# Optimization experiments

Measured on AMD Instinct MI355X. Metric: run time of the kernel, lower is better.

Reference implementation:

```python
import jax, jax.numpy as jnp
import numpy as np

EPS = 1e-5
NUM_HEADS = 4

# Spiking neuron: single-timestep LIF with threshold 1.0 (Heaviside forward,
# ATan surrogate gradient as in snntorch's default spike_grad).
@jax.custom_vjp
def spike(v):
    return (v >= 1.0).astype(v.dtype)

def _spike_fwd(v):
    return spike(v), v

def _spike_bwd(v, g):
    u = v - 1.0
    return (g / (1.0 + (jnp.pi * u) ** 2),)

spike.defvjp(_spike_fwd, _spike_bwd)

def layernorm(x, g, b):
    mu = jnp.mean(x, axis=-1, keepdims=True)
    var = jnp.var(x, axis=-1, keepdims=True)
    return (x - mu) * jax.lax.rsqrt(var + EPS) * g + b

def batchnorm(x, g, b):
    # BatchNorm1d applied on (B, C, N) == per-channel stats over (B, N) of (B, N, C)
    mu = jnp.mean(x, axis=(0, 1))
    var = jnp.var(x, axis=(0, 1))
    return (x - mu) * jax.lax.rsqrt(var + EPS) * g + b

def lin_bn_spike(x, w, g, b):
    # Linear (no bias) -> BatchNorm1d -> spiking neuron
    return spike(batchnorm(jnp.einsum('bnc,oc->bno', x, w), g, b))


def setup_inputs() -> dict:
    key = jax.random.key(0)
    ks = jax.random.split(key, 8)
    B, N, C = 8, 2048, 256
    Hid = 1024  # int(256 * 4.0)
    s = 0.02
    d = {
        'x': jax.random.normal(ks[0], (B, N, C), jnp.float32),
        'ln1_g': jnp.ones((C,), jnp.float32), 'ln1_b': jnp.zeros((C,), jnp.float32),
        'wq': jax.random.normal(ks[1], (C, C), jnp.float32) * s,
        'q_g': jnp.ones((C,), jnp.float32), 'q_b': jnp.zeros((C,), jnp.float32),
        'wk': jax.random.normal(ks[2], (C, C), jnp.float32) * s,
        'k_g': jnp.ones((C,), jnp.float32), 'k_b': jnp.zeros((C,), jnp.float32),
        'wv': jax.random.normal(ks[3], (C, C), jnp.float32) * s,
        'v_g': jnp.ones((C,), jnp.float32), 'v_b': jnp.zeros((C,), jnp.float32),
        'wo': jax.random.normal(ks[4], (C, C), jnp.float32) * s,
        'ln2_g': jnp.ones((C,), jnp.float32), 'ln2_b': jnp.zeros((C,), jnp.float32),
        'w1': jax.random.normal(ks[5], (Hid, C), jnp.float32) * s,
        'bn1_g': jnp.ones((Hid,), jnp.float32), 'bn1_b': jnp.zeros((Hid,), jnp.float32),
        'w2': jax.random.normal(ks[6], (C, Hid), jnp.float32) * s,
        'bn2_g': jnp.ones((C,), jnp.float32), 'bn2_b': jnp.zeros((C,), jnp.float32),
    }
    return d


def reference(x, ln1_g, ln1_b, wq, q_g, q_b, wk, k_g, k_b, wv, v_g, v_b, wo,
              ln2_g, ln2_b, w1, bn1_g, bn1_b, w2, bn2_g, bn2_b):
    B, N, C = x.shape
    H = NUM_HEADS
    D = C // H
    scale = D ** (-0.5)

    # --- Spiking self-attention on norm1(x) ---
    h = layernorm(x, ln1_g, ln1_b)
    q = lin_bn_spike(h, wq, q_g, q_b)
    k = lin_bn_spike(h, wk, k_g, k_b)
    v = lin_bn_spike(h, wv, v_g, v_b)
    qh = q.reshape(B, N, H, D).transpose(0, 2, 1, 3)
    kh = k.reshape(B, N, H, D).transpose(0, 2, 1, 3)
    vh = v.reshape(B, N, H, D).transpose(0, 2, 1, 3)
    attn = jnp.einsum('bhnd,bhmd->bhnm', qh, kh) * scale  # no softmax
    o = jnp.einsum('bhnm,bhmd->bhnd', attn, vh)
    o = o.transpose(0, 2, 1, 3).reshape(B, N, C)
    x = x + jnp.einsum('bnc,oc->bno', o, wo)

    # --- Spiking MLP on norm2(x) (dropout=0.0) ---
    h = layernorm(x, ln2_g, ln2_b)
    m = lin_bn_spike(h, w1, bn1_g, bn1_b)
    m = lin_bn_spike(m, w2, bn2_g, bn2_b)
    return x + m
```

## Files before the change

### kernel.cpp

```cpp
#include <hip/hip_runtime.h>
#include <cstddef>
#include <cstdint>

#define RR 16384
#define CC 256
#define NN 2048

typedef __attribute__((ext_vector_type(8))) _Float16 h8;
typedef __attribute__((ext_vector_type(4))) float float4v;
typedef unsigned short u16;

__device__ inline float h2f(u16 u) {
  return (float)__builtin_bit_cast(_Float16, u);
}
__device__ inline u16 f2h(float f) {
  return __builtin_bit_cast(u16, (_Float16)f);
}

__global__ __launch_bounds__(256) void ln_split(const float* __restrict__ x,
    const float* __restrict__ g, const float* __restrict__ b,
    u16* __restrict__ out) {
  const int wave = threadIdx.x >> 6, lane = threadIdx.x & 63;
  const int row = (blockIdx.x << 2) + wave;
  const float4 v = ((const float4*)(x + (size_t)row * CC))[lane];
  float s1 = v.x + v.y + v.z + v.w;
  float s2 = v.x * v.x + v.y * v.y + v.z * v.z + v.w * v.w;
#pragma unroll
  for (int o = 32; o > 0; o >>= 1) {
    s1 += __shfl_xor(s1, o);
    s2 += __shfl_xor(s2, o);
  }
  const float mu = s1 * (1.0f / CC);
  const float var = s2 * (1.0f / CC) - mu * mu;
  const float rs = 1.0f / sqrtf(var + 1e-5f);
  const float4 gg = ((const float4*)g)[lane];
  const float4 bb = ((const float4*)b)[lane];
  float o4[4];
  o4[0] = (v.x - mu) * rs * gg.x + bb.x;
  o4[1] = (v.y - mu) * rs * gg.y + bb.y;
  o4[2] = (v.z - mu) * rs * gg.z + bb.z;
  o4[3] = (v.w - mu) * rs * gg.w + bb.w;
  ushort4 hi, lo;
  hi.x = f2h(o4[0]); lo.x = f2h(o4[0] - h2f(hi.x));
  hi.y = f2h(o4[1]); lo.y = f2h(o4[1] - h2f(hi.y));
  hi.z = f2h(o4[2]); lo.z = f2h(o4[2] - h2f(hi.z));
  hi.w = f2h(o4[3]); lo.w = f2h(o4[3] - h2f(hi.w));
  *(ushort4*)(out + (size_t)row * 512 + (lane << 2)) = hi;
  *(ushort4*)(out + (size_t)row * 512 + 256 + (lane << 2)) = lo;
}

__global__ __launch_bounds__(256) void split_all(const float* __restrict__ wq,
    const float* __restrict__ wk, const float* __restrict__ wv,
    const float* __restrict__ wo, const float* __restrict__ w1,
    const float* __restrict__ w2, u16* __restrict__ Wqkv,
    u16* __restrict__ wo2, u16* __restrict__ w12, u16* __restrict__ w22) {
  const int bid = blockIdx.x;
  if (bid < 768) {
    const float* W = (bid < 256) ? wq : (bid < 512) ? wk : wv;
    const int rowoff = (bid >> 8) << 8;
    const int li = (bid & 255) * 256 + threadIdx.x;
    const int o = li >> 8, k = li & 255;
    const float w = W[li];
    const u16 h1 = f2h(w);
    const u16 h2 = f2h(w - h2f(h1));
    u16* base = Wqkv + (size_t)(o + rowoff) * 768;
    base[k] = h1; base[256 + k] = h1; base[512 + k] = h2;
  } else if (bid < 1024) {
    const int li = (bid - 768) * 256 + threadIdx.x;
    wo2[li] = f2h(wo[li]);
  } else if (bid < 2048) {
    const int li = (bid - 1024) * 256 + threadIdx.x;
    w12[li] = f2h(w1[li]);
  } else {
    const int li = (bid - 2048) * 256 + threadIdx.x;
    w22[li] = f2h(w2[li]);
  }
}

template <int BM, int BN, int WM, int WN, int STATS, int MINW, int OUTF16,
          int LNFUSE>
__global__ __launch_bounds__(512, MINW) void gemm_sp(
    const u16* __restrict__ A, int AW,
    const u16* __restrict__ W2, int K2,
    const float* __restrict__ resid, void* __restrict__ Yv, int O,
    float* __restrict__ p1, float* __restrict__ p2,
    const float* __restrict__ lng, const float* __restrict__ lnb,
    u16* __restrict__ h2out) {
  constexpr int FM = BM / (WM * 16);
  constexpr int FN = BN / (WN * 16);
  constexpr int LA = BM / 64;
  constexpr int LB = BN / 64;
  constexpr int NL = LA + LB;
  static_assert(WM * WN == 8, "8 waves");
  static_assert(NL == 3 || NL == 4 || NL == 5 || NL == 7 || NL == 8,
                "vmcnt literal");
  static_assert(!LNFUSE || (BM == 64 && BN == 256), "LNFUSE tile");
  __shared__ __align__(16) u16 As[2][BM * 64];
  __shared__ __align__(16) u16 Bs[2][BN * 64];
  const int tid = threadIdx.x;
  const int lane = tid & 63, wid = tid >> 6;
  const int wr = wid / WN, wc = wid % WN;
  const int gx = gridDim.x;
  const int lid = blockIdx.y * gx + blockIdx.x;
  const int chunk = (gx * gridDim.y) >> 3;
  const int nid = (lid & 7) * chunk + (lid >> 3);
  const int bx = nid % gx, by = nid / gx;
  const int r0 = by * BM, o0 = bx * BN;
  const int lrow = tid >> 3;
  const int lce = ((tid & 7) ^ ((tid >> 3) & 7)) << 3;

  auto STAGE = [&](int buf, int kAs, int k0s) {
#pragma unroll
    for (int i = 0; i < LA; ++i) {
      const u16* srcA = A + (size_t)(r0 + i * 64 + lrow) * AW + kAs + lce;
      __builtin_amdgcn_global_load_lds(
          (const __attribute__((address_space(1))) void*)srcA,
          (__attribute__((address_space(3))) void*)&As[buf][(i * 64 + wid * 8) * 64],
          16, 0, 0);
    }
#pragma unroll
    for (int i = 0; i < LB; ++i) {
      const u16* srcB = W2 + (size_t)(o0 + i * 64 + lrow) * K2 + k0s + lce;
      __builtin_amdgcn_global_load_lds(
          (const __attribute__((address_space(1))) void*)srcB,
          (__attribute__((address_space(3))) void*)&Bs[buf][(i * 64 + wid * 8) * 64],
          16, 0, 0);
    }
  };

  float4v acc[FM][FN] = {};
  STAGE(0, 0, 0);
  int kA = 0, cur = 0;
  for (int k0 = 0; k0 < K2; k0 += 64) {
    const int kAn = (kA + 64) & (AW - 1);
    if (k0 + 64 < K2) {
      STAGE(cur ^ 1, kAn, k0 + 64);
      if constexpr (NL == 3)
        asm volatile("s_waitcnt vmcnt(3)\n\ts_barrier" ::: "memory");
      else if constexpr (NL == 4)
        asm volatile("s_waitcnt vmcnt(4)\n\ts_barrier" ::: "memory");
      else if constexpr (NL == 5)
        asm volatile("s_waitcnt vmcnt(5)\n\ts_barrier" ::: "memory");
      else if constexpr (NL == 7)
        asm volatile("s_waitcnt vmcnt(7)\n\ts_barrier" ::: "memory");
      else
        asm volatile("s_waitcnt vmcnt(8)\n\ts_barrier" ::: "memory");
    } else {
      asm volatile("s_waitcnt vmcnt(0)\n\ts_barrier" ::: "memory");
    }
#pragma unroll
    for (int kk = 0; kk < 2; ++kk) {
      h8 a[FM], b[FN];
      const int ch0 = (kk << 2) + (lane >> 4);
      const int chs = ch0 ^ (lane & 7);
#pragma unroll
      for (int m = 0; m < FM; ++m) {
        const int R = wr * (FM * 16) + m * 16 + (lane & 15);
        a[m] = *(const h8*)&As[cur][R * 64 + chs * 8];
      }
#pragma unroll
      for (int n = 0; n < FN; ++n) {
        const int Rb = wc * (FN * 16) + n * 16 + (lane & 15);
        b[n] = *(const h8*)&Bs[cur][Rb * 64 + chs * 8];
      }
#pragma unroll
      for (int m = 0; m < FM; ++m)
#pragma unroll
        for (int n = 0; n < FN; ++n)
          acc[m][n] = __builtin_amdgcn_mfma_f32_16x16x32_f16(a[m], b[n], acc[m][n], 0, 0, 0);
    }
    asm volatile("s_waitcnt lgkmcnt(0)\n\ts_barrier" ::: "memory");
    kA = kAn; cur ^= 1;
  }
  const int crow = (lane >> 4) << 2, ccol = lane & 15;
  float* ft = (float*)Bs;
#pragma unroll
  for (int m = 0; m < FM; ++m)
#pragma unroll
    for (int n = 0; n < FN; ++n)
#pragma unroll
      for (int j = 0; j < 4; ++j) {
        const int lr = wr * (FM * 16) + (m << 4) + crow + j;
        const int lc = wc * (FN * 16) + (n << 4) + ccol;
        const size_t idx = (size_t)(r0 + lr) * O + o0 + lc;
        float v = acc[m][n][j];
        if constexpr (OUTF16) {
          ((u16*)Yv)[idx] = f2h(v);
        } else {
          if (resid) v += resid[idx];
          ((float*)Yv)[idx] = v;
        }
        if constexpr (LNFUSE) ft[lr * 256 + lc] = v;
      }
  if constexpr (LNFUSE) {
    __syncthreads();
    const int rr0 = wid << 3;
    const float4 gg = ((const float4*)lng)[lane];
    const float4 bb = ((const float4*)lnb)[lane];
#pragma unroll
    for (int rr = 0; rr < 8; ++rr) {
      const int r = rr0 + rr;
      const float4 v = ((const float4*)ft)[r * 64 + lane];
      float s1 = v.x + v.y + v.z + v.w;
      float s2 = v.x * v.x + v.y * v.y + v.z * v.z + v.w * v.w;
#pragma unroll
      for (int o = 32; o > 0; o >>= 1) {
        s1 += __shfl_xor(s1, o);
        s2 += __shfl_xor(s2, o);
      }
      const float mu = s1 * (1.0f / CC);
      const float var = s2 * (1.0f / CC) - mu * mu;
      const float rs = 1.0f / sqrtf(var + 1e-5f);
      ushort4 hh;
      hh.x = f2h((v.x - mu) * rs * gg.x + bb.x);
      hh.y = f2h((v.y - mu) * rs * gg.y + bb.y);
      hh.z = f2h((v.z - mu) * rs * gg.z + bb.z);
      hh.w = f2h((v.w - mu) * rs * gg.w + bb.w);
      *(ushort4*)(h2out + (size_t)(r0 + r) * 256 + (lane << 2)) = hh;
    }
  }
  if (STATS) {
    float s1[FN], s2[FN];
#pragma unroll
    for (int n = 0; n < FN; ++n) {
      s1[n] = 0.f; s2[n] = 0.f;
#pragma unroll
      for (int m = 0; m < FM; ++m)
#pragma unroll
        for (int j = 0; j < 4; ++j) {
          const float v = acc[m][n][j];
          s1[n] += v; s2[n] += v * v;
        }
    }
#pragma unroll
    for (int n = 0; n < FN; ++n) {
      s1[n] += __shfl_xor(s1[n], 16); s1[n] += __shfl_xor(s1[n], 32);
      s2[n] += __shfl_xor(s2[n], 16); s2[n] += __shfl_xor(s2[n], 32);
    }
    float* sb = (float*)As;
    __syncthreads();
    if (lane < 16) {
#pragma unroll
      for (int n = 0; n < FN; ++n) {
        const int cl = wc * (FN * 16) + n * 16 + lane;
        sb[wr * BN + cl] = s1[n];
        sb[WM * BN + wr * BN + cl] = s2[n];
      }
    }
    __syncthreads();
    if (tid < BN) {
      float a = 0.f, b = 0.f;
#pragma unroll
      for (int w = 0; w < WM; ++w) {
        a += sb[w * BN + tid];
        b += sb[WM * BN + w * BN + tid];
      }
      p1[(size_t)by * O + o0 + tid] = a;
      p2[(size_t)by * O + o0 + tid] = b;
    }
  }
}

__global__ __launch_bounds__(256) void bn_stats2(const float* __restrict__ p1,
    const float* __restrict__ p2, float* __restrict__ mu,
    float* __restrict__ rinv, int O, int npanels) {
  const int c0 = blockIdx.x << 6;
  const int c = threadIdx.x & 63;
  const int jg = threadIdx.x >> 6;
  float s1 = 0.f, s2 = 0.f;
#pragma unroll 4
  for (int j = jg; j < npanels; j += 4) {
    s1 += p1[(size_t)j * O + c0 + c];
    s2 += p2[(size_t)j * O + c0 + c];
  }
  __shared__ float sb[8][64];
  sb[jg][c] = s1;
  sb[4 + jg][c] = s2;
  __syncthreads();
  if (threadIdx.x < 64) {
    const float a = ((sb[0][c] + sb[1][c]) + (sb[2][c] + sb[3][c]));
    const float b = ((sb[4][c] + sb[5][c]) + (sb[6][c] + sb[7][c]));
    const float m = a * (1.0f / 16384.f);
    const float v = b * (1.0f / 16384.f) - m * m;
    mu[c0 + c] = m;
    rinv[c0 + c] = 1.0f / sqrtf(v + 1e-5f);
  }
}

__global__ __launch_bounds__(256) void bn_spike_h16(const u16* __restrict__ Y,
    const float* __restrict__ mu, const float* __restrict__ rinv,
    const float* __restrict__ g, const float* __restrict__ b,
    u16* __restrict__ S, int O) {
  const int i = blockIdx.x * 256 + threadIdx.x;
  const int c = (i << 2) & (O - 1);
  const ushort4 yh = ((const ushort4*)Y)[i];
  const float4 m4 = *(const float4*)(mu + c);
  const float4 r4 = *(const float4*)(rinv + c);
  const float4 g4 = *(const float4*)(g + c);
  const float4 b4 = *(const float4*)(b + c);
  ushort4 s;
  s.x = ((h2f(yh.x) - m4.x) * r4.x * g4.x + b4.x >= 1.0f) ? (u16)0x3C00 : (u16)0;
  s.y = ((h2f(yh.y) - m4.y) * r4.y * g4.y + b4.y >= 1.0f) ? (u16)0x3C00 : (u16)0;
  s.z = ((h2f(yh.z) - m4.z) * r4.z * g4.z + b4.z >= 1.0f) ? (u16)0x3C00 : (u16)0;
  s.w = ((h2f(yh.w) - m4.w) * r4.w * g4.w + b4.w >= 1.0f) ? (u16)0x3C00 : (u16)0;
  ((ushort4*)S)[i] = s;
}

__global__ __launch_bounds__(256) void bn_spike_add_h16(
    const u16* __restrict__ Y, const float* __restrict__ mu,
    const float* __restrict__ rinv, const float* __restrict__ g,
    const float* __restrict__ b, float* __restrict__ addOut, int O) {
  const int i = blockIdx.x * 256 + threadIdx.x;
  const int c = (i << 2) & (O - 1);
  const ushort4 yh = ((const ushort4*)Y)[i];
  const float4 m4 = *(const float4*)(mu + c);
  const float4 r4 = *(const float4*)(rinv + c);
  const float4 g4 = *(const float4*)(g + c);
  const float4 b4 = *(const float4*)(b + c);
  float4 o4 = ((const float4*)addOut)[i];
  o4.x += ((h2f(yh.x) - m4.x) * r4.x * g4.x + b4.x >= 1.0f) ? 1.0f : 0.0f;
  o4.y += ((h2f(yh.y) - m4.y) * r4.y * g4.y + b4.y >= 1.0f) ? 1.0f : 0.0f;
  o4.z += ((h2f(yh.z) - m4.z) * r4.z * g4.z + b4.z >= 1.0f) ? 1.0f : 0.0f;
  o4.w += ((h2f(yh.w) - m4.w) * r4.w * g4.w + b4.w >= 1.0f) ? 1.0f : 0.0f;
  ((float4*)addOut)[i] = o4;
}

__global__ __launch_bounds__(256) void attn_kv(const float* __restrict__ Yq,
    const float* __restrict__ mu, const float* __restrict__ rinv,
    const float* __restrict__ kg, const float* __restrict__ kb,
    const float* __restrict__ vg, const float* __restrict__ vb,
    float* __restrict__ Mpart) {
  const int bh = blockIdx.x, sp = blockIdx.y;
  const int b = bh >> 2, h = bh & 3;
  const int t = threadIdx.x;
  const int gq = t >> 6, e = t & 63;
  __shared__ float ks[16][64], vs[16][64];
  float acc[16] = {};
  const int lrow = t >> 4, lf = (t & 15) << 2;
  const int c = (h << 6) + lf;
  const int ck = 256 + c, cv = 512 + c;
  const float4 kmu = *(const float4*)(mu + ck);
  const float4 krv = *(const float4*)(rinv + ck);
  const float4 kg4 = *(const float4*)(kg + c);
  const float4 kb4 = *(const float4*)(kb + c);
  const float4 vmu = *(const float4*)(mu + cv);
  const float4 vrv = *(const float4*)(rinv + cv);
  const float4 vg4 = *(const float4*)(vg + c);
  const float4 vb4 = *(const float4*)(vb + c);
  for (int n0 = sp * 128; n0 < sp * 128 + 128; n0 += 16) {
    const size_t rowb = (size_t)(b * NN + n0 + lrow) * 768;
    const float4 kq = *(const float4*)(Yq + rowb + ck);
    const float4 vq = *(const float4*)(Yq + rowb + cv);
    __syncthreads();
    ks[lrow][lf + 0] = ((kq.x - kmu.x) * krv.x * kg4.x + kb4.x >= 1.0f) ? 1.f : 0.f;
    ks[lrow][lf + 1] = ((kq.y - kmu.y) * krv.y * kg4.y + kb4.y >= 1.0f) ? 1.f : 0.f;
    ks[lrow][lf + 2] = ((kq.z - kmu.z) * krv.z * kg4.z + kb4.z >= 1.0f) ? 1.f : 0.f;
    ks[lrow][lf + 3] = ((kq.w - kmu.w) * krv.w * kg4.w + kb4.w >= 1.0f) ? 1.f : 0.f;
    vs[lrow][lf + 0] = ((vq.x - vmu.x) * vrv.x * vg4.x + vb4.x >= 1.0f) ? 1.f : 0.f;
    vs[lrow][lf + 1] = ((vq.y - vmu.y) * vrv.y * vg4.y + vb4.y >= 1.0f) ? 1.f : 0.f;
    vs[lrow][lf + 2] = ((vq.z - vmu.z) * vrv.z * vg4.z + vb4.z >= 1.0f) ? 1.f : 0.f;
    vs[lrow][lf + 3] = ((vq.w - vmu.w) * vrv.w * vg4.w + vb4.w >= 1.0f) ? 1.f : 0.f;
    __syncthreads();
#pragma unroll
    for (int nn = 0; nn < 16; ++nn) {
      const float vv = vs[nn][e];
#pragma unroll
      for (int i = 0; i < 16; ++i) acc[i] += ks[nn][(gq << 4) + i] * vv;
    }
  }
  float* mp = Mpart + ((size_t)bh * 16 + sp) * 4096;
#pragma unroll
  for (int i = 0; i < 16; ++i) mp[((gq << 4) + i) * 64 + e] = acc[i];
}

__global__ __launch_bounds__(256) void attn_kv_reduce(
    const float* __restrict__ Mpart, float* __restrict__ M) {
  const int i = blockIdx.x * 256 + threadIdx.x;
  const int bh = i >> 12, j = i & 4095;
  float s = 0.f;
#pragma unroll
  for (int sp = 0; sp < 16; ++sp)
    s += Mpart[((size_t)bh * 16 + sp) * 4096 + j];
  M[i] = s;
}

__global__ __launch_bounds__(256) void attn_qm(const float* __restrict__ Yq,
    const float* __restrict__ mu, const float* __restrict__ rinv,
    const float* __restrict__ qg, const float* __restrict__ qb,
    const float* __restrict__ M, u16* __restrict__ O1) {
  const int h = blockIdx.x;
  const int r0 = blockIdx.y << 6;
  const int b = blockIdx.y >> 5;
  const int t = threadIdx.x;
  const int e = t & 63, rg = t >> 6;
  __shared__ float Ms[64][64];
  __shared__ float qs[64][64];
  const float* Mb = M + ((size_t)(b * 4 + h) << 12);
  for (int i = t; i < 4096; i += 256) ((float*)Ms)[i] = Mb[i];
  const int c = (h << 6) + e;
  const float qmu = mu[c], qrv = rinv[c], qgg = qg[c], qbb = qb[c];
  for (int rl = rg; rl < 64; rl += 4) {
    const float y = Yq[(size_t)(r0 + rl) * 768 + c];
    qs[rl][e] = ((y - qmu) * qrv * qgg + qbb >= 1.0f) ? 1.f : 0.f;
  }
  __syncthreads();
  for (int rl = rg; rl < 64; rl += 4) {
    float acc = 0.f;
#pragma unroll
    for (int d = 0; d < 64; ++d) acc += qs[rl][d] * Ms[d][e];
    O1[(size_t)(r0 + rl) * 256 + (h << 6) + e] = f2h(0.125f * acc);
  }
}

extern "C" void kernel_launch(void* const* d_in, const int* in_sizes, int n_in,
                              void* d_out, int out_size, void* d_ws,
                              size_t ws_size, hipStream_t stream) {
  const float* x    = (const float*)d_in[0];
  const float* ln1g = (const float*)d_in[1];
  const float* ln1b = (const float*)d_in[2];
  const float* wq   = (const float*)d_in[3];
  const float* qg   = (const float*)d_in[4];
  const float* qb   = (const float*)d_in[5];
  const float* wk   = (const float*)d_in[6];
  const float* kg   = (const float*)d_in[7];
  const float* kb   = (const float*)d_in[8];
  const float* wv   = (const float*)d_in[9];
  const float* vg   = (const float*)d_in[10];
  const float* vb   = (const float*)d_in[11];
  const float* wo   = (const float*)d_in[12];
  const float* ln2g = (const float*)d_in[13];
  const float* ln2b = (const float*)d_in[14];
  const float* w1   = (const float*)d_in[15];
  const float* b1g  = (const float*)d_in[16];
  const float* b1b  = (const float*)d_in[17];
  const float* w2   = (const float*)d_in[18];
  const float* b2g  = (const float*)d_in[19];
  const float* b2b  = (const float*)d_in[20];
  float* out = (float*)d_out;
  char* ws = (char*)d_ws;
  const size_t MB = 1u << 20;
  u16*   h1s   = (u16*)(ws);
  float* Yq    = (float*)(ws + 16 * MB);
  float* Mpart = (float*)(ws + 88 * MB);
  float* Mful  = (float*)(ws + 96 * MB);
  u16*   o16   = (u16*)(ws);
  u16*   h2_16 = (u16*)(ws + 16 * MB);
  u16*   Ym16  = (u16*)(ws + 32 * MB);
  u16*   Y2    = (u16*)(ws + 64 * MB);
  u16*   m1    = (u16*)(ws + 97 * MB);
  u16*   Wqkv  = (u16*)(ws + 129 * MB);
  u16*   wo2   = (u16*)(ws + 131 * MB);
  u16*   w12   = (u16*)(ws + 132 * MB);
  u16*   w22   = (u16*)(ws + 134 * MB);
  float* p1    = (float*)(ws + 135 * MB);
  float* p2    = (float*)(ws + 136 * MB);
  float* mu    = (float*)(ws + 137 * MB);
  float* rinv  = (float*)(ws + 137 * MB + 32768);

  const dim3 blk(256);
  const dim3 blk512(512);

  split_all<<<3072, blk, 0, stream>>>(wq, wk, wv, wo, w1, w2, Wqkv, wo2, w12, w22);

  ln_split<<<RR / 4, blk, 0, stream>>>(x, ln1g, ln1b, h1s);

  gemm_sp<128, 192, 2, 4, 1, 4, 0, 0><<<dim3(4, 128), blk512, 0, stream>>>(
      h1s, 512, Wqkv, 768, nullptr, Yq, 768, p1, p2, nullptr, nullptr, nullptr);

  bn_stats2<<<12, blk, 0, stream>>>(p1, p2, mu, rinv, 768, 128);

  attn_kv<<<dim3(32, 16), blk, 0, stream>>>(Yq, mu, rinv, kg, kb, vg, vb, Mpart);
  attn_kv_reduce<<<512, blk, 0, stream>>>(Mpart, Mful);
  attn_qm<<<dim3(4, RR / 64), blk, 0, stream>>>(Yq, mu, rinv, qg, qb, Mful, o16);

  gemm_sp<64, 256, 2, 4, 0, 4, 0, 1><<<dim3(1, 256), blk512, 0, stream>>>(
      o16, 256, wo2, 256, x, out, 256, nullptr, nullptr, ln2g, ln2b, h2_16);

  gemm_sp<128, 128, 2, 4, 1, 4, 1, 0><<<dim3(8, 128), blk512, 0, stream>>>(
      h2_16, 256, w12, 256, nullptr, Ym16, 1024, p1, p2, nullptr, nullptr,
      nullptr);
  bn_stats2<<<16, blk, 0, stream>>>(p1, p2, mu, rinv, 1024, 128);
  bn_spike_h16<<<16384, blk, 0, stream>>>(Ym16, mu, rinv, b1g, b1b, m1, 1024);

  gemm_sp<64, 128, 2, 4, 1, 4, 1, 0><<<dim3(2, 256), blk512, 0, stream>>>(
      m1, 1024, w22, 1024, nullptr, Y2, 256, p1, p2, nullptr, nullptr, nullptr);
  bn_stats2<<<4, blk, 0, stream>>>(p1, p2, mu, rinv, 256, 256);
  bn_spike_add_h16<<<4096, blk, 0, stream>>>(Y2, mu, rinv, b2g, b2b, out, 256);
}
```

Measured before the change: 172.8 us.

## Fuse BN1+spike into MLP second GEMM A-tile load path

Removes the standalone bn_spike_h16 pass over the 16384x1024 hidden activations. The second MLP GEMM now reads the fp16 pre-BN outputs and applies the folded per-channel scale/shift plus threshold while staging A into LDS. bn_stats2 is extended to precompute the scale and shift so the fused path needs only one FMA per element. This saves a full read and write of a 32MB intermediate and one launch, at the cost of extra ALU work and register pressure inside the GEMM's A-load path, which now goes through registers instead of direct-to-LDS.

```diff
diff --git a/kernel.cpp b/kernel.cpp
--- a/kernel.cpp
+++ b/kernel.cpp
@@ -8,6 +8,7 @@
 
 typedef __attribute__((ext_vector_type(8))) _Float16 h8;
 typedef __attribute__((ext_vector_type(4))) float float4v;
+typedef __attribute__((ext_vector_type(8))) unsigned short u16x8;
 typedef unsigned short u16;
 
 __device__ inline float h2f(u16 u) {
@@ -261,9 +262,160 @@
   }
 }
 
+__global__ __launch_bounds__(512, 4) void gemm_mlp2f(
+    const u16* __restrict__ A, const u16* __restrict__ W2,
+    const float* __restrict__ sc, const float* __restrict__ sh,
+    u16* __restrict__ Y, float* __restrict__ p1, float* __restrict__ p2) {
+  constexpr int BM = 64, BN = 128, WM = 2, WN = 4, K2 = 1024;
+  constexpr int FM = 2, FN = 2;
+  __shared__ __align__(16) u16 As[2][BM * 64];
+  __shared__ __align__(16) u16 Bs[2][BN * 64];
+  const int tid = threadIdx.x;
+  const int lane = tid & 63, wid = tid >> 6;
+  const int wr = wid / WN, wc = wid % WN;
+  const int gx = gridDim.x;
+  const int lid = blockIdx.y * gx + blockIdx.x;
+  const int chunk = (gx * gridDim.y) >> 3;
+  const int nid = (lid & 7) * chunk + (lid >> 3);
+  const int bx = nid % gx, by = nid / gx;
+  const int r0 = by * BM, o0 = bx * BN;
+  const int lrow = tid >> 3;
+  const int cs = (tid & 7) ^ (lrow & 7);
+
+  u16x8 a1, a2;
+  float4 c01, c11, s01, s11, c02, c12, s02, s12;
+  auto LOADA = [&](int k0s, u16x8& av, float4& c0, float4& c1, float4& s0,
+                   float4& s1) {
+    av = *(const u16x8*)(A + (size_t)(r0 + lrow) * 1024 + k0s + cs * 8);
+    const int ch = k0s + cs * 8;
+    c0 = *(const float4*)(sc + ch);
+    c1 = *(const float4*)(sc + ch + 4);
+    s0 = *(const float4*)(sh + ch);
+    s1 = *(const float4*)(sh + ch + 4);
+  };
+  auto STAGE_B = [&](int buf, int k0s) {
+#pragma unroll
+    for (int i = 0; i < 2; ++i) {
+      const u16* srcB = W2 + (size_t)(o0 + i * 64 + lrow) * K2 + k0s +
+                        (((tid & 7) ^ (lrow & 7)) << 3);
+      __builtin_amdgcn_global_load_lds(
+          (const __attribute__((address_space(1))) void*)srcB,
+          (__attribute__((address_space(3))) void*)&Bs[buf][(i * 64 + wid * 8) * 64],
+          16, 0, 0);
+    }
+  };
+  auto WRITEA = [&](int buf, u16x8 av, float4 c0, float4 c1, float4 s0,
+                    float4 s1) {
+    u16x8 sp;
+    sp[0] = (h2f(av[0]) * c0.x + s0.x >= 1.0f) ? (u16)0x3C00 : (u16)0;
+    sp[1] = (h2f(av[1]) * c0.y + s0.y >= 1.0f) ? (u16)0x3C00 : (u16)0;
+    sp[2] = (h2f(av[2]) * c0.z + s0.z >= 1.0f) ? (u16)0x3C00 : (u16)0;
+    sp[3] = (h2f(av[3]) * c0.w + s0.w >= 1.0f) ? (u16)0x3C00 : (u16)0;
+    sp[4] = (h2f(av[4]) * c1.x + s1.x >= 1.0f) ? (u16)0x3C00 : (u16)0;
+    sp[5] = (h2f(av[5]) * c1.y + s1.y >= 1.0f) ? (u16)0x3C00 : (u16)0;
+    sp[6] = (h2f(av[6]) * c1.z + s1.z >= 1.0f) ? (u16)0x3C00 : (u16)0;
+    sp[7] = (h2f(av[7]) * c1.w + s1.w >= 1.0f) ? (u16)0x3C00 : (u16)0;
+    *(u16x8*)&As[buf][lrow * 64 + (tid & 7) * 8] = sp;
+  };
+
+  float4v acc[FM][FN] = {};
+  LOADA(0, a1, c01, c11, s01, s11);
+  STAGE_B(0, 0);
+  int cur = 0;
+  for (int k0 = 0; k0 < K2; k0 += 64) {
+    if (k0 + 64 < K2) {
+      LOADA(k0 + 64, a2, c02, c12, s02, s12);
+      STAGE_B(cur ^ 1, k0 + 64);
+      asm volatile("s_waitcnt vmcnt(7)\n\ts_barrier" ::: "memory");
+    } else {
+      asm volatile("s_waitcnt vmcnt(0)\n\ts_barrier" ::: "memory");
+    }
+    WRITEA(cur, a1, c01, c11, s01, s11);
+    asm volatile("s_waitcnt lgkmcnt(0)\n\ts_barrier" ::: "memory");
+#pragma unroll
+    for (int kk = 0; kk < 2; ++kk) {
+      h8 a[FM], b[FN];
+      const int ch0 = (kk << 2) + (lane >> 4);
+      const int chs = ch0 ^ (lane & 7);
+#pragma unroll
+      for (int m = 0; m < FM; ++m) {
+        const int R = wr * 32 + m * 16 + (lane & 15);
+        a[m] = *(const h8*)&As[cur][R * 64 + chs * 8];
+      }
+#pragma unroll
+      for (int n = 0; n < FN; ++n) {
+        const int Rb = wc * 32 + n * 16 + (lane & 15);
+        b[n] = *(const h8*)&Bs[cur][Rb * 64 + chs * 8];
+      }
+#pragma unroll
+      for (int m = 0; m < FM; ++m)
+#pragma unroll
+        for (int n = 0; n < FN; ++n)
+          acc[m][n] = __builtin_amdgcn_mfma_f32_16x16x32_f16(a[m], b[n], acc[m][n], 0, 0, 0);
+    }
+    asm volatile("s_waitcnt lgkmcnt(0)\n\ts_barrier" ::: "memory");
+    cur ^= 1;
+    a1 = a2; c01 = c02; c11 = c12; s01 = s02; s11 = s12;
+  }
+  const int crow = (lane >> 4) << 2, ccol = lane & 15;
+#pragma unroll
+  for (int m = 0; m < FM; ++m)
+#pragma unroll
+    for (int n = 0; n < FN; ++n)
+#pragma unroll
+      for (int j = 0; j < 4; ++j) {
+        const size_t idx =
+            (size_t)(r0 + wr * 32 + (m << 4) + crow + j) * 256 +
+            o0 + wc * 32 + (n << 4) + ccol;
+        Y[idx] = f2h(acc[m][n][j]);
+      }
+  {
+    float s1[FN], s2[FN];
+#pragma unroll
+    for (int n = 0; n < FN; ++n) {
+      s1[n] = 0.f; s2[n] = 0.f;
+#pragma unroll
+      for (int m = 0; m < FM; ++m)
+#pragma unroll
+        for (int j = 0; j < 4; ++j) {
+          const float v = acc[m][n][j];
+          s1[n] += v; s2[n] += v * v;
+        }
+    }
+#pragma unroll
+    for (int n = 0; n < FN; ++n) {
+      s1[n] += __shfl_xor(s1[n], 16); s1[n] += __shfl_xor(s1[n], 32);
+      s2[n] += __shfl_xor(s2[n], 16); s2[n] += __shfl_xor(s2[n], 32);
+    }
+    float* sb = (float*)As;
+    __syncthreads();
+    if (lane < 16) {
+#pragma unroll
+      for (int n = 0; n < FN; ++n) {
+        const int cl = wc * 32 + n * 16 + lane;
+        sb[wr * BN + cl] = s1[n];
+        sb[WM * BN + wr * BN + cl] = s2[n];
+      }
+    }
+    __syncthreads();
+    if (tid < BN) {
+      float a = 0.f, b = 0.f;
+#pragma unroll
+      for (int w = 0; w < WM; ++w) {
+        a += sb[w * BN + tid];
+        b += sb[WM * BN + w * BN + tid];
+      }
+      p1[(size_t)by * 256 + o0 + tid] = a;
+      p2[(size_t)by * 256 + o0 + tid] = b;
+    }
+  }
+}
+
 __global__ __launch_bounds__(256) void bn_stats2(const float* __restrict__ p1,
     const float* __restrict__ p2, float* __restrict__ mu,
-    float* __restrict__ rinv, int O, int npanels) {
+    float* __restrict__ rinv, int O, int npanels,
+    const float* __restrict__ g, const float* __restrict__ b,
+    float* __restrict__ sc, float* __restrict__ sh) {
   const int c0 = blockIdx.x << 6;
   const int c = threadIdx.x & 63;
   const int jg = threadIdx.x >> 6;
@@ -279,31 +431,18 @@
   __syncthreads();
   if (threadIdx.x < 64) {
     const float a = ((sb[0][c] + sb[1][c]) + (sb[2][c] + sb[3][c]));
-    const float b = ((sb[4][c] + sb[5][c]) + (sb[6][c] + sb[7][c]));
+    const float bb = ((sb[4][c] + sb[5][c]) + (sb[6][c] + sb[7][c]));
     const float m = a * (1.0f / 16384.f);
-    const float v = b * (1.0f / 16384.f) - m * m;
+    const float v = bb * (1.0f / 16384.f) - m * m;
+    const float rv = 1.0f / sqrtf(v + 1e-5f);
     mu[c0 + c] = m;
-    rinv[c0 + c] = 1.0f / sqrtf(v + 1e-5f);
-  }
-}
-
-__global__ __launch_bounds__(256) void bn_spike_h16(const u16* __restrict__ Y,
-    const float* __restrict__ mu, const float* __restrict__ rinv,
-    const float* __restrict__ g, const float* __restrict__ b,
-    u16* __restrict__ S, int O) {
-  const int i = blockIdx.x * 256 + threadIdx.x;
-  const int c = (i << 2) & (O - 1);
-  const ushort4 yh = ((const ushort4*)Y)[i];
-  const float4 m4 = *(const float4*)(mu + c);
-  const float4 r4 = *(const float4*)(rinv + c);
-  const float4 g4 = *(const float4*)(g + c);
-  const float4 b4 = *(const float4*)(b + c);
-  ushort4 s;
-  s.x = ((h2f(yh.x) - m4.x) * r4.x * g4.x + b4.x >= 1.0f) ? (u16)0x3C00 : (u16)0;
-  s.y = ((h2f(yh.y) - m4.y) * r4.y * g4.y + b4.y >= 1.0f) ? (u16)0x3C00 : (u16)0;
-  s.z = ((h2f(yh.z) - m4.z) * r4.z * g4.z + b4.z >= 1.0f) ? (u16)0x3C00 : (u16)0;
-  s.w = ((h2f(yh.w) - m4.w) * r4.w * g4.w + b4.w >= 1.0f) ? (u16)0x3C00 : (u16)0;
-  ((ushort4*)S)[i] = s;
+    rinv[c0 + c] = rv;
+    if (sc) {
+      const float scale = rv * g[c0 + c];
+      sc[c0 + c] = scale;
+      sh[c0 + c] = b[c0 + c] - m * scale;
+    }
+  }
 }
 
 __global__ __launch_bounds__(256) void bn_spike_add_h16(
@@ -447,7 +586,6 @@
   u16*   h2_16 = (u16*)(ws + 16 * MB);
   u16*   Ym16  = (u16*)(ws + 32 * MB);
   u16*   Y2    = (u16*)(ws + 64 * MB);
-  u16*   m1    = (u16*)(ws + 97 * MB);
   u16*   Wqkv  = (u16*)(ws + 129 * MB);
   u16*   wo2   = (u16*)(ws + 131 * MB);
   u16*   w12   = (u16*)(ws + 132 * MB);
@@ -456,6 +594,8 @@
   float* p2    = (float*)(ws + 136 * MB);
   float* mu    = (float*)(ws + 137 * MB);
   float* rinv  = (float*)(ws + 137 * MB + 32768);
+  float* sc1   = (float*)(ws + 137 * MB + 65536);
+  float* sh1   = (float*)(ws + 137 * MB + 65536 + 4096);
 
   const dim3 blk(256);
   const dim3 blk512(512);
@@ -467,7 +607,8 @@
   gemm_sp<128, 192, 2, 4, 1, 4, 0, 0><<<dim3(4, 128), blk512, 0, stream>>>(
       h1s, 512, Wqkv, 768, nullptr, Yq, 768, p1, p2, nullptr, nullptr, nullptr);
 
-  bn_stats2<<<12, blk, 0, stream>>>(p1, p2, mu, rinv, 768, 128);
+  bn_stats2<<<12, blk, 0, stream>>>(p1, p2, mu, rinv, 768, 128, nullptr,
+                                    nullptr, nullptr, nullptr);
 
   attn_kv<<<dim3(32, 16), blk, 0, stream>>>(Yq, mu, rinv, kg, kb, vg, vb, Mpart);
   attn_kv_reduce<<<512, blk, 0, stream>>>(Mpart, Mful);
@@ -479,11 +620,12 @@
   gemm_sp<128, 128, 2, 4, 1, 4, 1, 0><<<dim3(8, 128), blk512, 0, stream>>>(
       h2_16, 256, w12, 256, nullptr, Ym16, 1024, p1, p2, nullptr, nullptr,
       nullptr);
-  bn_stats2<<<16, blk, 0, stream>>>(p1, p2, mu, rinv, 1024, 128);
-  bn_spike_h16<<<16384, blk, 0, stream>>>(Ym16, mu, rinv, b1g, b1b, m1, 1024);
-
-  gemm_sp<64, 128, 2, 4, 1, 4, 1, 0><<<dim3(2, 256), blk512, 0, stream>>>(
-      m1, 1024, w22, 1024, nullptr, Y2, 256, p1, p2, nullptr, nullptr, nullptr);
-  bn_stats2<<<4, blk, 0, stream>>>(p1, p2, mu, rinv, 256, 256);
+  bn_stats2<<<16, blk, 0, stream>>>(p1, p2, mu, rinv, 1024, 128, b1g, b1b,
+                                    sc1, sh1);
+
+  gemm_mlp2f<<<dim3(2, 256), blk512, 0, stream>>>(Ym16, w22, sc1, sh1, Y2,
+                                                  p1, p2);
+  bn_stats2<<<4, blk, 0, stream>>>(p1, p2, mu, rinv, 256, 256, nullptr,
+                                   nullptr, nullptr, nullptr);
   bn_spike_add_h16<<<4096, blk, 0, stream>>>(Y2, mu, rinv, b2g, b2b, out, 256);
 }
```

Result: faster. 166.5 us (-3.7%).
